# Optimization experiments

Measured on AMD Instinct MI355X. Metric: run time of the kernel, lower is better.

## Reference

```python
import jax, jax.numpy as jnp
import numpy as np

BN_EPS = 1e-5


def _guide_net(fullres, w1, b1, bn_gamma, bn_beta, bn_mean, bn_var, w2, b2):
    # two 1x1 convs == channel matmuls
    x = jnp.einsum('nchw,oc->nohw', fullres, w1[:, :, 0, 0]) + b1[None, :, None, None]
    inv = bn_gamma / jnp.sqrt(bn_var + BN_EPS)
    x = (x - bn_mean[None, :, None, None]) * inv[None, :, None, None] + bn_beta[None, :, None, None]
    x = jax.nn.relu(x)
    g = jnp.einsum('nchw,oc->nohw', x, w2[:, :, 0, 0]) + b2[None, :, None, None]
    return jax.nn.sigmoid(g)  # [N,1,H,W] in (0,1)


def _slice_one(grid_n, guide_n):
    # grid_n: [C,D,h,w]; guide_n: [H,W]; trilinear grid_sample, align_corners=True.
    C, D, h, w = grid_n.shape
    H, W = guide_n.shape
    # normalized coords in torch code map exactly to voxel coords [0, size-1]
    gz = guide_n * (D - 1)                      # per-pixel depth coord [H,W]
    z0f = jnp.floor(gz)
    tz = (gz - z0f)[None, :, :]                 # [1,H,W]
    z0 = jnp.clip(z0f, 0, D - 1).astype(jnp.int32)
    z1 = jnp.clip(z0f + 1, 0, D - 1).astype(jnp.int32)
    gy = jnp.linspace(0.0, h - 1.0, H)
    y0f = jnp.floor(gy)
    ty = (gy - y0f)[None, :, None]              # [1,H,1]
    y0 = jnp.clip(y0f, 0, h - 1).astype(jnp.int32)[:, None]
    y1 = jnp.clip(y0f + 1, 0, h - 1).astype(jnp.int32)[:, None]
    gx = jnp.linspace(0.0, w - 1.0, W)
    x0f = jnp.floor(gx)
    tx = (gx - x0f)[None, None, :]              # [1,1,W]
    x0 = jnp.clip(x0f, 0, w - 1).astype(jnp.int32)[None, :]
    x1 = jnp.clip(x0f + 1, 0, w - 1).astype(jnp.int32)[None, :]

    def g(z, y, x):
        # z:[H,W], y:[H,1], x:[1,W] -> broadcast gather -> [C,H,W]
        return grid_n[:, z, y, x]

    def lerp_xy(z):
        a = g(z, y0, x0) * (1 - tx) + g(z, y0, x1) * tx
        b = g(z, y1, x0) * (1 - tx) + g(z, y1, x1) * tx
        return a * (1 - ty) + b * ty

    return lerp_xy(z0) * (1 - tz) + lerp_xy(z1) * tz  # [C,H,W]


def _apply_coeffs(coeff, fullres):
    # coeff: [N,12,H,W]; rows (0:3,+3), (4:7,+7), (8:11,+11)
    N, _, H, W = coeff.shape
    A = coeff[:, jnp.array([0, 1, 2, 4, 5, 6, 8, 9, 10])].reshape(N, 3, 3, H, W)
    bias = coeff[:, jnp.array([3, 7, 11])]
    return jnp.einsum('nkchw,nchw->nkhw', A, fullres) + bias


def setup_inputs() -> dict:
    key = jax.random.key(0)
    ks = jax.random.split(key, 10)
    N, H, W = 2, 1080, 1920
    return {
        'fullres': jax.random.uniform(ks[0], (N, 3, H, W), jnp.float32),
        'bilateral_grid': jax.random.normal(ks[1], (N, 12, 8, 16, 16), jnp.float32),
        'w1': jax.random.normal(ks[2], (16, 3, 1, 1), jnp.float32) * 0.2,
        'b1': jax.random.normal(ks[3], (16,), jnp.float32) * 0.1,
        'bn_gamma': jax.random.uniform(ks[4], (16,), jnp.float32, 0.5, 1.5),
        'bn_beta': jax.random.normal(ks[5], (16,), jnp.float32) * 0.1,
        'bn_mean': jax.random.normal(ks[6], (16,), jnp.float32) * 0.1,
        'bn_var': jax.random.uniform(ks[7], (16,), jnp.float32, 0.5, 1.5),
        'w2': jax.random.normal(ks[8], (1, 16, 1, 1), jnp.float32) * 0.2,
        'b2': jax.random.normal(ks[9], (1,), jnp.float32) * 0.1,
    }


def reference(fullres, bilateral_grid, w1, b1, bn_gamma, bn_beta, bn_mean, bn_var, w2, b2):
    guide = _guide_net(fullres, w1, b1, bn_gamma, bn_beta, bn_mean, bn_var, w2, b2)  # [N,1,H,W]
    coeff = jax.vmap(_slice_one)(bilateral_grid, guide[:, 0])                         # [N,12,H,W]
    return _apply_coeffs(coeff, fullres)                                              # [N,3,H,W]
```

## Files before the change

### kernel.cpp

```cpp
#include <hip/hip_runtime.h>
#include <hip/hip_bf16.h>
#include <math.h>

#define HWV (1080 * 1920)
#define NPIX (2 * HWV)

typedef _Float16 half2 __attribute__((ext_vector_type(2)));
typedef __fp16   pk2   __attribute__((ext_vector_type(2)));
union U32H2 { unsigned u; half2 h; pk2 p; };

__global__ void prep_kernel(const float* __restrict__ grid,
                            const float* __restrict__ w1,
                            const float* __restrict__ b1,
                            const float* __restrict__ gamma,
                            const float* __restrict__ beta,
                            const float* __restrict__ mean,
                            const float* __restrict__ var,
                            const float* __restrict__ w2,
                            const float* __restrict__ b2,
                            float* __restrict__ wsg,
                            float* __restrict__ wsw) {
    int i = blockIdx.x * blockDim.x + threadIdx.x;
    if (i < 2 * 12 * 8 * 16 * 16) {
        int c = i % 12;
        int t = i / 12;
        int z = t % 8;  t /= 8;
        int x = t % 16; t /= 16;
        int y = t % 16;
        int n = t / 16;
        wsg[i] = grid[n * 24576 + c * 2048 + z * 256 + y * 16 + x];
    }
    if (i < 16) {
        float inv = gamma[i] / sqrtf(var[i] + 1e-5f);
        wsw[i]      = w1[i * 3 + 0] * inv;
        wsw[16 + i] = w1[i * 3 + 1] * inv;
        wsw[32 + i] = w1[i * 3 + 2] * inv;
        wsw[48 + i] = (b1[i] - mean[i]) * inv + beta[i];
        wsw[64 + i] = w2[i];
    }
    if (i == 0) wsw[80] = b2[0];
    if (i < 8) {
        int c0 = 2 * i, c1 = 2 * i + 1;
        float inv0 = gamma[c0] / sqrtf(var[c0] + 1e-5f);
        float inv1 = gamma[c1] / sqrtf(var[c1] + 1e-5f);
        unsigned* wp = (unsigned*)(wsw + 84);
        U32H2 t;
        t.p = __builtin_amdgcn_cvt_pkrtz(w1[c0*3+0] * inv0, w1[c1*3+0] * inv1);
        wp[i * 4 + 0] = t.u;
        t.p = __builtin_amdgcn_cvt_pkrtz(w1[c0*3+1] * inv0, w1[c1*3+1] * inv1);
        wp[i * 4 + 1] = t.u;
        t.p = __builtin_amdgcn_cvt_pkrtz(w1[c0*3+2] * inv0, w1[c1*3+2] * inv1);
        wp[i * 4 + 2] = t.u;
        t.p = __builtin_amdgcn_cvt_pkrtz((b1[c0] - mean[c0]) * inv0 + beta[c0],
                                         (b1[c1] - mean[c1]) * inv1 + beta[c1]);
        wp[i * 4 + 3] = t.u;
    }
}

__global__ __launch_bounds__(512, 8) void fused_kernel(
        const float* __restrict__ fullres,
        const float* __restrict__ wsg,
        const float* __restrict__ wsw,
        float* __restrict__ out) {
    __shared__ unsigned slo[6][9][4];
    __shared__ unsigned shi[6][9][2];

    const int tid = threadIdx.x;
    const int n   = blockIdx.z;
    const int y   = blockIdx.y;
    const int xs  = blockIdx.x * 512;
    const int x   = xs + tid;
    const bool act = (x < 1920);

    const int p  = y * 1920 + min(x, 1919);
    const float* fr = fullres + n * 3 * HWV + p;
    float r = fr[0];
    float g = fr[HWV];
    float b = fr[2 * HWV];

    const int a = (int)((float)xs * (15.0f / 1919.0f));
    {
        float gy = (float)y * (15.0f / 1079.0f);
        float y0f = floorf(gy);
        float ty = gy - y0f;
        int y0 = min((int)y0f, 15);
        int y1 = min(y0 + 1, 15);
        const float* gbase = wsg + n * 24576;
        if (tid < 324) {
            int k = tid / 54;
            int rem = tid - k * 54;
            int z = rem / 6;
            int j = rem - z * 6;
            int zz = min(z, 7);
            int xc = min(a + k, 15);
            const float2 v0 = *(const float2*)(gbase + ((y0 * 16 + xc) * 8 + zz) * 12 + 2 * j);
            const float2 v1 = *(const float2*)(gbase + ((y1 * 16 + xc) * 8 + zz) * 12 + 2 * j);
            float e0 = fmaf(ty, v1.x - v0.x, v0.x);
            float e1 = fmaf(ty, v1.y - v0.y, v0.y);
            U32H2 t;
            t.p = __builtin_amdgcn_cvt_pkrtz(e0, e1);
            if (j < 4) slo[k][z][j] = t.u;
            else       shi[k][z][j - 4] = t.u;
        }
    }
    __syncthreads();

    if (!act) return;

    U32H2 rr, gg, bb;
    rr.p = __builtin_amdgcn_cvt_pkrtz(r, r);
    gg.p = __builtin_amdgcn_cvt_pkrtz(g, g);
    bb.p = __builtin_amdgcn_cvt_pkrtz(b, b);
    const unsigned* wp = (const unsigned*)(wsw + 84);
    const half2 zero = {(_Float16)0.0f, (_Float16)0.0f};
    float acc = wsw[80];
#pragma unroll
    for (int c2 = 0; c2 < 8; ++c2) {
        U32H2 wr, wg, wb, wbs;
        wr.u  = wp[c2 * 4 + 0];
        wg.u  = wp[c2 * 4 + 1];
        wb.u  = wp[c2 * 4 + 2];
        wbs.u = wp[c2 * 4 + 3];
        half2 h = wr.h * rr.h + (wg.h * gg.h + (wb.h * bb.h + wbs.h));
        h = __builtin_elementwise_max(h, zero);
        acc = fmaf((float)h.x, wsw[64 + 2 * c2],     acc);
        acc = fmaf((float)h.y, wsw[64 + 2 * c2 + 1], acc);
    }
    float e = __expf(-acc);
    float guide = __builtin_amdgcn_rcpf(1.0f + e);

    float gz = guide * 7.0f;
    float z0f = floorf(gz);
    float tz = gz - z0f;
    int z0 = min((int)z0f, 7);
    int z1 = z0 + 1;

    float gx = (float)x * (15.0f / 1919.0f);
    float x0f = floorf(gx);
    float tx = gx - x0f;
    int x0 = (int)x0f;
    int k0 = x0 - a;
    int k1 = min(x0 + 1, 15) - a;

    float wx0 = 1.0f - tx, wx1 = tx;
    float wz0 = 1.0f - tz, wz1 = tz;

    U32H2 w00h, w01h, w10h, w11h;
    w00h.p = __builtin_amdgcn_cvt_pkrtz(wx0 * wz0, wx0 * wz0);
    w01h.p = __builtin_amdgcn_cvt_pkrtz(wx0 * wz1, wx0 * wz1);
    w10h.p = __builtin_amdgcn_cvt_pkrtz(wx1 * wz0, wx1 * wz0);
    w11h.p = __builtin_amdgcn_cvt_pkrtz(wx1 * wz1, wx1 * wz1);

    const uint4 A0 = *(const uint4*)&slo[k0][z0][0];
    const uint4 A1 = *(const uint4*)&slo[k0][z1][0];
    const uint4 B0 = *(const uint4*)&slo[k1][z0][0];
    const uint4 B1 = *(const uint4*)&slo[k1][z1][0];
    const uint2 C0 = *(const uint2*)&shi[k0][z0][0];
    const uint2 C1 = *(const uint2*)&shi[k0][z1][0];
    const uint2 D0 = *(const uint2*)&shi[k1][z0][0];
    const uint2 D1 = *(const uint2*)&shi[k1][z1][0];

    unsigned a0j[6] = {A0.x, A0.y, A0.z, A0.w, C0.x, C0.y};
    unsigned a1j[6] = {A1.x, A1.y, A1.z, A1.w, C1.x, C1.y};
    unsigned b0j[6] = {B0.x, B0.y, B0.z, B0.w, D0.x, D0.y};
    unsigned b1j[6] = {B1.x, B1.y, B1.z, B1.w, D1.x, D1.y};

    half2 hc[6];
#pragma unroll
    for (int j = 0; j < 6; ++j) {
        U32H2 ua0, ua1, ub0, ub1;
        ua0.u = a0j[j]; ua1.u = a1j[j]; ub0.u = b0j[j]; ub1.u = b1j[j];
        half2 h = w00h.h * ua0.h + (w01h.h * ua1.h);
        h = w10h.h * ub0.h + h;
        h = w11h.h * ub1.h + h;
        hc[j] = h;
    }

    float* op = out + n * 3 * HWV + p;
    op[0]       = fmaf((float)hc[0].x, r, fmaf((float)hc[0].y, g,
                  fmaf((float)hc[1].x, b, (float)hc[1].y)));
    op[HWV]     = fmaf((float)hc[2].x, r, fmaf((float)hc[2].y, g,
                  fmaf((float)hc[3].x, b, (float)hc[3].y)));
    op[2 * HWV] = fmaf((float)hc[4].x, r, fmaf((float)hc[4].y, g,
                  fmaf((float)hc[5].x, b, (float)hc[5].y)));
}

extern "C" void kernel_launch(void* const* d_in, const int* in_sizes, int n_in,
                              void* d_out, int out_size, void* d_ws, size_t ws_size,
                              hipStream_t stream) {
    const float* fullres = (const float*)d_in[0];
    const float* grid    = (const float*)d_in[1];
    const float* w1      = (const float*)d_in[2];
    const float* b1      = (const float*)d_in[3];
    const float* gamma   = (const float*)d_in[4];
    const float* beta    = (const float*)d_in[5];
    const float* mean    = (const float*)d_in[6];
    const float* var     = (const float*)d_in[7];
    const float* w2      = (const float*)d_in[8];
    const float* b2      = (const float*)d_in[9];
    float* out = (float*)d_out;

    float* wsg = (float*)d_ws;
    float* wsw = wsg + 49152;

    prep_kernel<<<192, 256, 0, stream>>>(grid, w1, b1, gamma, beta, mean, var,
                                         w2, b2, wsg, wsw);

    dim3 grid_dim(4, 1080, 2);
    fused_kernel<<<grid_dim, 512, 0, stream>>>(fullres, wsg, wsw, out);
}
```

Before: 33.37 us.

## Process two pixels per thread and read grid directly without transpose

Each thread now handles two adjacent pixels, using float2 loads and stores and half2 lanes that carry the two pixels instead of two channels. Blocks cover 1024 columns, so the shared slice grows to 9 x-cells, and it is built straight from the original grid layout. This lets the grid-transpose prep kernel shrink to a tiny weight-only kernel. The aim is to cut launch and prep overhead, halve the number of blocks and per-block slice builds, and widen memory accesses. In exchange, each thread uses more registers and the slice build now does scattered scalar loads.

New measurement: 32.25 us. 1.03x faster.

```diff
diff --git a/kernel.cpp b/kernel.cpp
--- a/kernel.cpp
+++ b/kernel.cpp
@@ -3,80 +3,52 @@
 #include <math.h>
 
 #define HWV (1080 * 1920)
-#define NPIX (2 * HWV)
 
 typedef _Float16 half2 __attribute__((ext_vector_type(2)));
 typedef __fp16   pk2   __attribute__((ext_vector_type(2)));
 union U32H2 { unsigned u; half2 h; pk2 p; };
 
-__global__ void prep_kernel(const float* __restrict__ grid,
-                            const float* __restrict__ w1,
-                            const float* __restrict__ b1,
-                            const float* __restrict__ gamma,
-                            const float* __restrict__ beta,
-                            const float* __restrict__ mean,
-                            const float* __restrict__ var,
-                            const float* __restrict__ w2,
-                            const float* __restrict__ b2,
-                            float* __restrict__ wsg,
-                            float* __restrict__ wsw) {
-    int i = blockIdx.x * blockDim.x + threadIdx.x;
-    if (i < 2 * 12 * 8 * 16 * 16) {
-        int c = i % 12;
-        int t = i / 12;
-        int z = t % 8;  t /= 8;
-        int x = t % 16; t /= 16;
-        int y = t % 16;
-        int n = t / 16;
-        wsg[i] = grid[n * 24576 + c * 2048 + z * 256 + y * 16 + x];
-    }
+__global__ void prep_w(const float* __restrict__ w1, const float* __restrict__ b1,
+                       const float* __restrict__ gamma, const float* __restrict__ beta,
+                       const float* __restrict__ mean, const float* __restrict__ var,
+                       const float* __restrict__ w2, const float* __restrict__ b2,
+                       float* __restrict__ wsw) {
+    int i = threadIdx.x;
     if (i < 16) {
         float inv = gamma[i] / sqrtf(var[i] + 1e-5f);
-        wsw[i]      = w1[i * 3 + 0] * inv;
-        wsw[16 + i] = w1[i * 3 + 1] * inv;
-        wsw[32 + i] = w1[i * 3 + 2] * inv;
-        wsw[48 + i] = (b1[i] - mean[i]) * inv + beta[i];
+        float wr = w1[i*3+0] * inv, wg = w1[i*3+1] * inv, wb = w1[i*3+2] * inv;
+        float bs = (b1[i] - mean[i]) * inv + beta[i];
         wsw[64 + i] = w2[i];
+        unsigned* wp = (unsigned*)(wsw + 84);
+        U32H2 t;
+        t.p = __builtin_amdgcn_cvt_pkrtz(wr, wr); wp[i*4+0] = t.u;
+        t.p = __builtin_amdgcn_cvt_pkrtz(wg, wg); wp[i*4+1] = t.u;
+        t.p = __builtin_amdgcn_cvt_pkrtz(wb, wb); wp[i*4+2] = t.u;
+        t.p = __builtin_amdgcn_cvt_pkrtz(bs, bs); wp[i*4+3] = t.u;
     }
     if (i == 0) wsw[80] = b2[0];
-    if (i < 8) {
-        int c0 = 2 * i, c1 = 2 * i + 1;
-        float inv0 = gamma[c0] / sqrtf(var[c0] + 1e-5f);
-        float inv1 = gamma[c1] / sqrtf(var[c1] + 1e-5f);
-        unsigned* wp = (unsigned*)(wsw + 84);
-        U32H2 t;
-        t.p = __builtin_amdgcn_cvt_pkrtz(w1[c0*3+0] * inv0, w1[c1*3+0] * inv1);
-        wp[i * 4 + 0] = t.u;
-        t.p = __builtin_amdgcn_cvt_pkrtz(w1[c0*3+1] * inv0, w1[c1*3+1] * inv1);
-        wp[i * 4 + 1] = t.u;
-        t.p = __builtin_amdgcn_cvt_pkrtz(w1[c0*3+2] * inv0, w1[c1*3+2] * inv1);
-        wp[i * 4 + 2] = t.u;
-        t.p = __builtin_amdgcn_cvt_pkrtz((b1[c0] - mean[c0]) * inv0 + beta[c0],
-                                         (b1[c1] - mean[c1]) * inv1 + beta[c1]);
-        wp[i * 4 + 3] = t.u;
-    }
 }
 
 __global__ __launch_bounds__(512, 8) void fused_kernel(
         const float* __restrict__ fullres,
-        const float* __restrict__ wsg,
+        const float* __restrict__ grid,
         const float* __restrict__ wsw,
         float* __restrict__ out) {
-    __shared__ unsigned slo[6][9][4];
-    __shared__ unsigned shi[6][9][2];
+    __shared__ unsigned slo[9][9][4];
+    __shared__ unsigned shi[9][9][2];
 
     const int tid = threadIdx.x;
     const int n   = blockIdx.z;
     const int y   = blockIdx.y;
-    const int xs  = blockIdx.x * 512;
-    const int x   = xs + tid;
+    const int xs  = blockIdx.x * 1024;
+    const int x   = xs + 2 * tid;
     const bool act = (x < 1920);
 
-    const int p  = y * 1920 + min(x, 1919);
+    const int p = y * 1920 + min(x, 1918);
     const float* fr = fullres + n * 3 * HWV + p;
-    float r = fr[0];
-    float g = fr[HWV];
-    float b = fr[2 * HWV];
+    float2 R = *(const float2*)(fr);
+    float2 G = *(const float2*)(fr + HWV);
+    float2 B = *(const float2*)(fr + 2 * HWV);
 
     const int a = (int)((float)xs * (15.0f / 1919.0f));
     {
@@ -85,18 +57,21 @@
         float ty = gy - y0f;
         int y0 = min((int)y0f, 15);
         int y1 = min(y0 + 1, 15);
-        const float* gbase = wsg + n * 24576;
-        if (tid < 324) {
-            int k = tid / 54;
-            int rem = tid - k * 54;
-            int z = rem / 6;
-            int j = rem - z * 6;
-            int zz = min(z, 7);
-            int xc = min(a + k, 15);
-            const float2 v0 = *(const float2*)(gbase + ((y0 * 16 + xc) * 8 + zz) * 12 + 2 * j);
-            const float2 v1 = *(const float2*)(gbase + ((y1 * 16 + xc) * 8 + zz) * 12 + 2 * j);
-            float e0 = fmaf(ty, v1.x - v0.x, v0.x);
-            float e1 = fmaf(ty, v1.y - v0.y, v0.y);
+        const int dy = (y1 - y0) * 16;
+        const float* gb = grid + n * 24576 + y0 * 16;
+        if (tid < 486) {
+            int j   = tid / 81;
+            int rem = tid - j * 81;
+            int z   = rem / 9;
+            int k   = rem - z * 9;
+            int zz  = min(z, 7);
+            int xc  = min(a + k, 15);
+            const float* q0 = gb + (2 * j) * 2048 + zz * 256 + xc;
+            const float* q1 = q0 + 2048;
+            float v00 = q0[0], v01 = q0[dy];
+            float v10 = q1[0], v11 = q1[dy];
+            float e0 = fmaf(ty, v01 - v00, v00);
+            float e1 = fmaf(ty, v11 - v10, v10);
             U32H2 t;
             t.p = __builtin_amdgcn_cvt_pkrtz(e0, e1);
             if (j < 4) slo[k][z][j] = t.u;
@@ -108,81 +83,91 @@
     if (!act) return;
 
     U32H2 rr, gg, bb;
-    rr.p = __builtin_amdgcn_cvt_pkrtz(r, r);
-    gg.p = __builtin_amdgcn_cvt_pkrtz(g, g);
-    bb.p = __builtin_amdgcn_cvt_pkrtz(b, b);
+    rr.p = __builtin_amdgcn_cvt_pkrtz(R.x, R.y);
+    gg.p = __builtin_amdgcn_cvt_pkrtz(G.x, G.y);
+    bb.p = __builtin_amdgcn_cvt_pkrtz(B.x, B.y);
     const unsigned* wp = (const unsigned*)(wsw + 84);
     const half2 zero = {(_Float16)0.0f, (_Float16)0.0f};
-    float acc = wsw[80];
+    float b2s = wsw[80];
+    float acc0 = b2s, acc1 = b2s;
 #pragma unroll
-    for (int c2 = 0; c2 < 8; ++c2) {
-        U32H2 wr, wg, wb, wbs;
-        wr.u  = wp[c2 * 4 + 0];
-        wg.u  = wp[c2 * 4 + 1];
-        wb.u  = wp[c2 * 4 + 2];
-        wbs.u = wp[c2 * 4 + 3];
-        half2 h = wr.h * rr.h + (wg.h * gg.h + (wb.h * bb.h + wbs.h));
+    for (int c = 0; c < 16; ++c) {
+        U32H2 wr, wg, wb, bs;
+        wr.u = wp[4*c+0]; wg.u = wp[4*c+1]; wb.u = wp[4*c+2]; bs.u = wp[4*c+3];
+        half2 h = wr.h * rr.h + (wg.h * gg.h + (wb.h * bb.h + bs.h));
         h = __builtin_elementwise_max(h, zero);
-        acc = fmaf((float)h.x, wsw[64 + 2 * c2],     acc);
-        acc = fmaf((float)h.y, wsw[64 + 2 * c2 + 1], acc);
+        float w2c = wsw[64 + c];
+        acc0 = fmaf((float)h.x, w2c, acc0);
+        acc1 = fmaf((float)h.y, w2c, acc1);
     }
-    float e = __expf(-acc);
-    float guide = __builtin_amdgcn_rcpf(1.0f + e);
 
-    float gz = guide * 7.0f;
-    float z0f = floorf(gz);
-    float tz = gz - z0f;
-    int z0 = min((int)z0f, 7);
-    int z1 = z0 + 1;
+    float accv[2] = {acc0, acc1};
+    float rv[2] = {R.x, R.y}, gv[2] = {G.x, G.y}, bv[2] = {B.x, B.y};
+    float outr[2], outg[2], outb[2];
 
-    float gx = (float)x * (15.0f / 1919.0f);
-    float x0f = floorf(gx);
-    float tx = gx - x0f;
-    int x0 = (int)x0f;
-    int k0 = x0 - a;
-    int k1 = min(x0 + 1, 15) - a;
+#pragma unroll
+    for (int q = 0; q < 2; ++q) {
+        float e = __expf(-accv[q]);
+        float guide = __builtin_amdgcn_rcpf(1.0f + e);
+        float gz = guide * 7.0f;
+        float z0f = floorf(gz);
+        float tz = gz - z0f;
+        int z0 = min((int)z0f, 7);
+        int z1 = z0 + 1;
 
-    float wx0 = 1.0f - tx, wx1 = tx;
-    float wz0 = 1.0f - tz, wz1 = tz;
+        float gx = (float)(x + q) * (15.0f / 1919.0f);
+        float x0f = floorf(gx);
+        float tx = gx - x0f;
+        int x0 = (int)x0f;
+        int k0 = x0 - a;
+        int k1 = min(x0 + 1, 15) - a;
 
-    U32H2 w00h, w01h, w10h, w11h;
-    w00h.p = __builtin_amdgcn_cvt_pkrtz(wx0 * wz0, wx0 * wz0);
-    w01h.p = __builtin_amdgcn_cvt_pkrtz(wx0 * wz1, wx0 * wz1);
-    w10h.p = __builtin_amdgcn_cvt_pkrtz(wx1 * wz0, wx1 * wz0);
-    w11h.p = __builtin_amdgcn_cvt_pkrtz(wx1 * wz1, wx1 * wz1);
+        float wx0 = 1.0f - tx, wx1 = tx;
+        float wz0 = 1.0f - tz, wz1 = tz;
 
-    const uint4 A0 = *(const uint4*)&slo[k0][z0][0];
-    const uint4 A1 = *(const uint4*)&slo[k0][z1][0];
-    const uint4 B0 = *(const uint4*)&slo[k1][z0][0];
-    const uint4 B1 = *(const uint4*)&slo[k1][z1][0];
-    const uint2 C0 = *(const uint2*)&shi[k0][z0][0];
-    const uint2 C1 = *(const uint2*)&shi[k0][z1][0];
-    const uint2 D0 = *(const uint2*)&shi[k1][z0][0];
-    const uint2 D1 = *(const uint2*)&shi[k1][z1][0];
+        U32H2 w00h, w01h, w10h, w11h;
+        w00h.p = __builtin_amdgcn_cvt_pkrtz(wx0 * wz0, wx0 * wz0);
+        w01h.p = __builtin_amdgcn_cvt_pkrtz(wx0 * wz1, wx0 * wz1);
+        w10h.p = __builtin_amdgcn_cvt_pkrtz(wx1 * wz0, wx1 * wz0);
+        w11h.p = __builtin_amdgcn_cvt_pkrtz(wx1 * wz1, wx1 * wz1);
 
-    unsigned a0j[6] = {A0.x, A0.y, A0.z, A0.w, C0.x, C0.y};
-    unsigned a1j[6] = {A1.x, A1.y, A1.z, A1.w, C1.x, C1.y};
-    unsigned b0j[6] = {B0.x, B0.y, B0.z, B0.w, D0.x, D0.y};
-    unsigned b1j[6] = {B1.x, B1.y, B1.z, B1.w, D1.x, D1.y};
+        const uint4 A0 = *(const uint4*)&slo[k0][z0][0];
+        const uint4 A1 = *(const uint4*)&slo[k0][z1][0];
+        const uint4 B0 = *(const uint4*)&slo[k1][z0][0];
+        const uint4 B1 = *(const uint4*)&slo[k1][z1][0];
+        const uint2 C0 = *(const uint2*)&shi[k0][z0][0];
+        const uint2 C1 = *(const uint2*)&shi[k0][z1][0];
+        const uint2 D0 = *(const uint2*)&shi[k1][z0][0];
+        const uint2 D1 = *(const uint2*)&shi[k1][z1][0];
 
-    half2 hc[6];
+        unsigned a0j[6] = {A0.x, A0.y, A0.z, A0.w, C0.x, C0.y};
+        unsigned a1j[6] = {A1.x, A1.y, A1.z, A1.w, C1.x, C1.y};
+        unsigned b0j[6] = {B0.x, B0.y, B0.z, B0.w, D0.x, D0.y};
+        unsigned b1j[6] = {B1.x, B1.y, B1.z, B1.w, D1.x, D1.y};
+
+        half2 hc[6];
 #pragma unroll
-    for (int j = 0; j < 6; ++j) {
-        U32H2 ua0, ua1, ub0, ub1;
-        ua0.u = a0j[j]; ua1.u = a1j[j]; ub0.u = b0j[j]; ub1.u = b1j[j];
-        half2 h = w00h.h * ua0.h + (w01h.h * ua1.h);
-        h = w10h.h * ub0.h + h;
-        h = w11h.h * ub1.h + h;
-        hc[j] = h;
+        for (int j = 0; j < 6; ++j) {
+            U32H2 ua0, ua1, ub0, ub1;
+            ua0.u = a0j[j]; ua1.u = a1j[j]; ub0.u = b0j[j]; ub1.u = b1j[j];
+            half2 h = w00h.h * ua0.h + (w01h.h * ua1.h);
+            h = w10h.h * ub0.h + h;
+            h = w11h.h * ub1.h + h;
+            hc[j] = h;
+        }
+
+        outr[q] = fmaf((float)hc[0].x, rv[q], fmaf((float)hc[0].y, gv[q],
+                  fmaf((float)hc[1].x, bv[q], (float)hc[1].y)));
+        outg[q] = fmaf((float)hc[2].x, rv[q], fmaf((float)hc[2].y, gv[q],
+                  fmaf((float)hc[3].x, bv[q], (float)hc[3].y)));
+        outb[q] = fmaf((float)hc[4].x, rv[q], fmaf((float)hc[4].y, gv[q],
+                  fmaf((float)hc[5].x, bv[q], (float)hc[5].y)));
     }
 
     float* op = out + n * 3 * HWV + p;
-    op[0]       = fmaf((float)hc[0].x, r, fmaf((float)hc[0].y, g,
-                  fmaf((float)hc[1].x, b, (float)hc[1].y)));
-    op[HWV]     = fmaf((float)hc[2].x, r, fmaf((float)hc[2].y, g,
-                  fmaf((float)hc[3].x, b, (float)hc[3].y)));
-    op[2 * HWV] = fmaf((float)hc[4].x, r, fmaf((float)hc[4].y, g,
-                  fmaf((float)hc[5].x, b, (float)hc[5].y)));
+    *(float2*)(op)           = make_float2(outr[0], outr[1]);
+    *(float2*)(op + HWV)     = make_float2(outg[0], outg[1]);
+    *(float2*)(op + 2 * HWV) = make_float2(outb[0], outb[1]);
 }
 
 extern "C" void kernel_launch(void* const* d_in, const int* in_sizes, int n_in,
@@ -200,12 +185,10 @@
     const float* b2      = (const float*)d_in[9];
     float* out = (float*)d_out;
 
-    float* wsg = (float*)d_ws;
-    float* wsw = wsg + 49152;
+    float* wsw = (float*)d_ws;
 
-    prep_kernel<<<192, 256, 0, stream>>>(grid, w1, b1, gamma, beta, mean, var,
-                                         w2, b2, wsg, wsw);
+    prep_w<<<1, 64, 0, stream>>>(w1, b1, gamma, beta, mean, var, w2, b2, wsw);
 
-    dim3 grid_dim(4, 1080, 2);
-    fused_kernel<<<grid_dim, 512, 0, stream>>>(fullres, wsg, wsw, out);
+    dim3 grid_dim(2, 1080, 2);
+    fused_kernel<<<grid_dim, 512, 0, stream>>>(fullres, grid, wsw, out);
 }
```
